# Kernel optimization log

Hardware: AMD Instinct MI355X
Metric: run time of the kernel (lower is better)

Reference implementation:

```python
import jax, jax.numpy as jnp
import numpy as np

F8_MAX = 448.0  # float8_e4m3fn max
F4_MAX = 6.0    # fp4 e2m1 max
BLOCK = 16      # NVFP4 scaling block size along K

# representable |values| of fp4 e2m1 and midpoints for nearest rounding
_LEVELS = jnp.array([0.0, 0.5, 1.0, 1.5, 2.0, 3.0, 4.0, 6.0], dtype=jnp.float32)
_MIDS = (_LEVELS[:-1] + _LEVELS[1:]) * 0.5


def _e2m1_round(a):
    # round-to-nearest fp4 e2m1 value, sign-magnitude
    s = jnp.sign(a)
    m = jnp.clip(jnp.abs(a), 0.0, F4_MAX)
    idx = jnp.searchsorted(_MIDS, m, side='left')
    return s * jnp.take(_LEVELS, idx)


def _e4m3(x):
    # quantize to float8 e4m3 and dequantize back to fp32
    return jnp.clip(x, -F8_MAX, F8_MAX).astype(jnp.float8_e4m3fn).astype(jnp.float32)


def nvfp4_fake_quant(x, s2):
    # x: [..., K]; s2: scalar global scale = 448*6/global_amax
    shp = x.shape
    K = shp[-1]
    xb = x.reshape(shp[:-1] + (K // BLOCK, BLOCK))  # [..., K/16, 16]
    amax = jnp.max(jnp.abs(xb), axis=-1, keepdims=True)
    sf = _e4m3(amax * s2 / F4_MAX)          # stored per-block fp8 scale (cutlass_vec)
    scale = sf / s2                          # per-block dequant scale in real units
    safe = jnp.where(scale > 0.0, scale, 1.0)
    q = _e2m1_round(xb / safe)               # fp4 codes (as values)
    deq = jnp.where(scale > 0.0, q * scale, 0.0)
    return deq.reshape(shp)


def setup_inputs() -> dict:
    key = jax.random.key(0)
    kx, kw, kb, ks = jax.random.split(key, 4)
    K, N = 4096, 4096
    x = jax.random.normal(kx, (4, 2048, K), dtype=jnp.float32)
    weight = jax.random.uniform(kw, (N, K), dtype=jnp.float32)
    bias = jax.random.uniform(kb, (N,), dtype=jnp.float32)
    # fp4_global_scale of a rand(1, K) tensor, as done in the module __init__
    dummy = jax.random.uniform(ks, (1, K), dtype=jnp.float32)
    s_in2 = ((F8_MAX * F4_MAX) / jnp.max(jnp.abs(dummy))).reshape(1)
    return {'x': x, 'weight': weight, 'bias': bias, 's_in2': s_in2}


def reference(x, weight, bias, s_in2):
    s2_in = s_in2.reshape(())
    s2_w = (F8_MAX * F4_MAX) / jnp.max(jnp.abs(weight))  # fp4_global_scale(weight)
    x_dq = nvfp4_fake_quant(x, s2_in)        # fake-quant activations
    w_dq = nvfp4_fake_quant(weight, s2_w)    # dequantized fp4 weight (stored at init)
    # F.linear: [b,s,k] @ [n,k]^T + bias
    return jnp.einsum('bsk,nk->bsn', x_dq, w_dq) + bias
```

## Files before the change

### kernel.cpp

```cpp
#include <hip/hip_runtime.h>
#include <hip/hip_bf16.h>

typedef __attribute__((ext_vector_type(8))) short short8;
typedef __attribute__((ext_vector_type(8))) unsigned short ushort8;
typedef __attribute__((ext_vector_type(4))) float f32x4;
typedef unsigned short ushort;

#define K_DIM 4096
#define N_DIM 4096
#define BK 64
#define NT (K_DIM / BK)


__device__ __forceinline__ float e4m3_rne(float v) {
    if (v >= 0.015625f) {
        unsigned u = __float_as_uint(v);
        unsigned lsb = (u >> 20) & 1u;
        u = (u + 0x7FFFFu + lsb) & 0xFFF00000u;
        return __uint_as_float(u);
    }
    return rintf(v * 512.0f) * 0.001953125f;
}

__device__ __forceinline__ float e2m1_level(float m) {
    float lv = 0.0f;
    lv = (m > 0.25f) ? 0.5f : lv;
    lv = (m > 0.75f) ? 1.0f : lv;
    lv = (m > 1.25f) ? 1.5f : lv;
    lv = (m > 1.75f) ? 2.0f : lv;
    lv = (m > 2.5f)  ? 3.0f : lv;
    lv = (m > 3.5f)  ? 4.0f : lv;
    lv = (m > 5.0f)  ? 6.0f : lv;
    return lv;
}

__device__ __forceinline__ ushort f32_to_bf16_bits(float f) {
    unsigned u = __float_as_uint(f);
    return (ushort)((u + 0x7FFFu + ((u >> 16) & 1u)) >> 16);
}


__global__ void wamax_kernel(const float* __restrict__ w, unsigned* amax_bits, int n4) {
    float m = 0.f;
    const f32x4* w4 = (const f32x4*)w;
    for (int i = blockIdx.x * blockDim.x + threadIdx.x; i < n4; i += gridDim.x * blockDim.x) {
        f32x4 v = w4[i];
        m = fmaxf(m, fmaxf(fmaxf(fabsf(v.x), fabsf(v.y)), fmaxf(fabsf(v.z), fabsf(v.w))));
    }
#pragma unroll
    for (int off = 32; off >= 1; off >>= 1)
        m = fmaxf(m, __shfl_down(m, off));
    __shared__ float red[4];
    const int lane = threadIdx.x & 63, wv = threadIdx.x >> 6;
    if (lane == 0) red[wv] = m;
    __syncthreads();
    if (threadIdx.x == 0) {
        m = fmaxf(fmaxf(red[0], red[1]), fmaxf(red[2], red[3]));
        atomicMax(amax_bits, __float_as_uint(m));
    }
}

__global__ void quant16_kernel(const float* __restrict__ src,
                               const float* __restrict__ s2_ptr,
                               const unsigned* __restrict__ amax_bits,
                               ushort* __restrict__ dst, int nblk) {
    int t = blockIdx.x * blockDim.x + threadIdx.x;
    if (t >= nblk) return;
    float s2;
    if (s2_ptr) s2 = *s2_ptr;
    else        s2 = 2688.0f / __uint_as_float(*amax_bits);

    const f32x4* s = (const f32x4*)src + (size_t)t * 4;
    float vals[16];
    f32x4 v0 = s[0], v1 = s[1], v2 = s[2], v3 = s[3];
#pragma unroll
    for (int i = 0; i < 4; ++i) {
        vals[i] = v0[i]; vals[4 + i] = v1[i]; vals[8 + i] = v2[i]; vals[12 + i] = v3[i];
    }
    float amax = 0.f;
#pragma unroll
    for (int i = 0; i < 16; ++i) amax = fmaxf(amax, fabsf(vals[i]));

    float sf = e4m3_rne(fminf(amax * s2 / 6.0f, 448.0f));
    float scale = sf / s2;

    ushort8 o0, o1;
    if (scale > 0.f) {
#pragma unroll
        for (int i = 0; i < 16; ++i) {
            float r = vals[i] / scale;
            float m = fminf(fabsf(r), 6.0f);
            float q = copysignf(e2m1_level(m), r);
            ushort b = f32_to_bf16_bits(q * scale);
            if (i < 8) o0[i] = b; else o1[i - 8] = b;
        }
    } else {
#pragma unroll
        for (int i = 0; i < 8; ++i) { o0[i] = 0; o1[i] = 0; }
    }
    ushort8* d8 = (ushort8*)(dst + (size_t)t * 16);
    d8[0] = o0;
    d8[1] = o1;
}


__device__ __forceinline__ void gload16(const ushort* g, ushort* l) {
    __builtin_amdgcn_global_load_lds(
        (const __attribute__((address_space(1))) void*)g,
        (__attribute__((address_space(3))) void*)l, 16, 0, 0);
}

#define VM4 asm volatile("s_waitcnt vmcnt(4)" ::: "memory")
#define VM2 asm volatile("s_waitcnt vmcnt(2)" ::: "memory")
#define VM0 asm volatile("s_waitcnt vmcnt(0)" ::: "memory")
#define BAR asm volatile("s_barrier" ::: "memory")

__global__ __launch_bounds__(512, 2) void gemm8(
    const ushort* __restrict__ Aq, const ushort* __restrict__ Bq,
    const float* __restrict__ bias, float* __restrict__ C) {
    __shared__ ushort lds[2 * 32768];

    const int tid  = threadIdx.x;
    const int lane = tid & 63;
    const int wave = tid >> 6;
    const int wr = wave >> 2;
    const int wc = wave & 3;

    const int swz = blockIdx.x;
    const int grp = swz >> 8, lcl = swz & 255;
    const int by = grp * 16 + (lcl & 15);
    const int bx = lcl >> 4;
    const int bm = by * 256, bn = bx * 256;

    const int r0  = tid >> 3;
    const int cg0 = ((tid & 7) - r0) & 7;
    const ushort* sA = Aq + (size_t)(bm + r0) * K_DIM + cg0 * 8;
    const ushort* sB = Bq + (size_t)(bn + r0) * K_DIM + cg0 * 8;
    ushort* dst0 = &lds[tid * 8];

    const int rowA = wr * 64 + (lane & 15);
    const int rowB = wc * 32 + (lane & 15);
    const int ksl  = lane >> 4;
    const int baseA[2] = { rowA * 64 + ((((ksl) + rowA) & 7) << 3),
                           rowA * 64 + (((4 + ksl + rowA) & 7) << 3) };
    const int baseB[2] = { 16384 + rowB * 64 + ((((ksl) + rowB) & 7) << 3),
                           16384 + rowB * 64 + (((4 + ksl + rowB) & 7) << 3) };

    f32x4 acc[8][4];
#pragma unroll
    for (int m = 0; m < 8; ++m)
#pragma unroll
        for (int n = 0; n < 4; ++n) acc[m][n] = (f32x4)(0.f);

    short8 af[4][2], bfr[4][2];

#define SA0(t) { const size_t ko = (size_t)(t) * BK; ushort* d = dst0 + ((t) & 1) * 32768;         \
    gload16(sA + ko, d); gload16(sA + (size_t)64 * K_DIM + ko, d + 4096); }
#define SA1(t) { const size_t ko = (size_t)(t) * BK; ushort* d = dst0 + ((t) & 1) * 32768 + 8192;  \
    gload16(sA + (size_t)128 * K_DIM + ko, d); gload16(sA + (size_t)192 * K_DIM + ko, d + 4096); }
#define SB0(t) { const size_t ko = (size_t)(t) * BK; ushort* d = dst0 + ((t) & 1) * 32768 + 16384; \
    gload16(sB + ko, d); gload16(sB + (size_t)64 * K_DIM + ko, d + 4096); }
#define SB1(t) { const size_t ko = (size_t)(t) * BK; ushort* d = dst0 + ((t) & 1) * 32768 + 24576; \
    gload16(sB + (size_t)128 * K_DIM + ko, d); gload16(sB + (size_t)192 * K_DIM + ko, d + 4096); }

#define READ_A(mh, Lb)                                                        \
    _Pragma("unroll") for (int m = 0; m < 4; ++m) {                           \
        af[m][0] = *(const short8*)((Lb) + (mh) * 8192 + m * 1024 + baseA[0]); \
        af[m][1] = *(const short8*)((Lb) + (mh) * 8192 + m * 1024 + baseA[1]); }
#define READ_B(nh, Lb)                                                        \
    _Pragma("unroll") for (int n = 0; n < 2; ++n) {                           \
        bfr[(nh)*2 + n][0] = *(const short8*)((Lb) + (nh) * 8192 + n * 1024 + baseB[0]); \
        bfr[(nh)*2 + n][1] = *(const short8*)((Lb) + (nh) * 8192 + n * 1024 + baseB[1]); }

#define MM(m0, n0)                                                            \
    __builtin_amdgcn_s_setprio(1);                                            \
    _Pragma("unroll") for (int m = 0; m < 4; ++m)                             \
    _Pragma("unroll") for (int n = 0; n < 2; ++n)                             \
    _Pragma("unroll") for (int ks = 0; ks < 2; ++ks)                          \
        acc[(m0) + m][(n0) + n] = __builtin_amdgcn_mfma_f32_16x16x32_bf16(    \
            af[m][ks], bfr[(n0) + n][ks], acc[(m0) + m][(n0) + n], 0, 0, 0);  \
    __builtin_amdgcn_s_setprio(0);

    SA0(0); SB0(0); SB1(0); SA1(0);
    VM4; BAR;

#pragma unroll 1
    for (int t = 0; t < NT - 1; ++t) {
        const ushort* Lb = &lds[(t & 1) * 32768];
        READ_A(0, Lb); READ_B(0, Lb);
        SA0(t + 1);
        VM4; BAR;
        MM(0, 0);
        BAR;
        READ_B(1, Lb);
        SB0(t + 1);
        VM4; BAR;
        MM(0, 2);
        BAR;
        READ_A(1, Lb);
        SB1(t + 1);
        BAR;
        MM(4, 0);
        BAR;
        SA1(t + 1);
        VM4; BAR;
        MM(4, 2);
        BAR;
    }
    {
        const ushort* Lb = &lds[((NT - 1) & 1) * 32768];
        READ_A(0, Lb); READ_B(0, Lb);
        VM2; BAR;
        MM(0, 0);
        BAR;
        READ_B(1, Lb);
        VM0; BAR;
        MM(0, 2);
        BAR;
        READ_A(1, Lb);
        BAR;
        MM(4, 0);
        BAR;
        BAR;
        MM(4, 2);
        BAR;
    }

    const int fq = lane >> 4, fr = lane & 15;
    const int colb = bn + wc * 32 + fr;
    float bv[4];
#pragma unroll
    for (int n = 0; n < 4; ++n) bv[n] = bias[colb + (n >> 1) * 128 + (n & 1) * 16];
#pragma unroll
    for (int m = 0; m < 8; ++m)
#pragma unroll
        for (int r = 0; r < 4; ++r) {
            const int row = bm + (m >> 2) * 128 + wr * 64 + (m & 3) * 16 + fq * 4 + r;
            float* Cr = C + (size_t)row * N_DIM + colb;
#pragma unroll
            for (int n = 0; n < 4; ++n)
                Cr[(n >> 1) * 128 + (n & 1) * 16] = acc[m][n][r] + bv[n];
        }
#undef SA0
#undef SA1
#undef SB0
#undef SB1
#undef READ_A
#undef READ_B
#undef MM
}


extern "C" void kernel_launch(void* const* d_in, const int* in_sizes, int n_in,
                              void* d_out, int out_size, void* d_ws, size_t ws_size,
                              hipStream_t stream) {
    const float* x     = (const float*)d_in[0];
    const float* w     = (const float*)d_in[1];
    const float* bias  = (const float*)d_in[2];
    const float* s_in2 = (const float*)d_in[3];
    float* out = (float*)d_out;

    const int M = in_sizes[0] / K_DIM;

    unsigned* amax_bits = (unsigned*)d_ws;
    ushort* xq = (ushort*)((char*)d_ws + 256);
    ushort* wq = (ushort*)((char*)d_ws + 256 + (size_t)M * K_DIM * 2);

    hipMemsetAsync(amax_bits, 0, 4, stream);
    wamax_kernel<<<1024, 256, 0, stream>>>(w, amax_bits, (N_DIM * K_DIM) / 4);

    const int nblk_x = (M * K_DIM) / 16;
    quant16_kernel<<<nblk_x / 256, 256, 0, stream>>>(x, s_in2, nullptr, xq, nblk_x);
    const int nblk_w = (N_DIM * K_DIM) / 16;
    quant16_kernel<<<nblk_w / 256, 256, 0, stream>>>(w, nullptr, amax_bits, wq, nblk_w);

    const int nwg = (M / 256) * (N_DIM / 256);
    gemm8<<<nwg, 512, 0, stream>>>(xq, wq, bias, out);
}
```

Before: 298.6 us.

## Double-buffer register fragments and prefetch next tile's LDS reads during MFMA

Splits A/B register fragments into separate low/high halves so the next k-tile's first fragments are read from LDS while the last MFMA quarter of the current tile runs. Replaces several full barriers with fine-grained lgkmcnt waits, which cuts the number of s_barrier stalls per iteration. This raises register pressure under the 512-thread, 2-block launch bounds. The reduced barrier set also risks LDS read/write hazards if the async global-to-LDS writes race with reads of the buffer being consumed.

```diff
diff --git a/kernel.cpp b/kernel.cpp
--- a/kernel.cpp
+++ b/kernel.cpp
@@ -113,6 +113,9 @@
 #define VM4 asm volatile("s_waitcnt vmcnt(4)" ::: "memory")
 #define VM2 asm volatile("s_waitcnt vmcnt(2)" ::: "memory")
 #define VM0 asm volatile("s_waitcnt vmcnt(0)" ::: "memory")
+#define LG4 asm volatile("s_waitcnt lgkmcnt(4)" ::: "memory")
+#define LG8 asm volatile("s_waitcnt lgkmcnt(8)" ::: "memory")
+#define LG0 asm volatile("s_waitcnt lgkmcnt(0)" ::: "memory")
 #define BAR asm volatile("s_barrier" ::: "memory")
 
 __global__ __launch_bounds__(512, 2) void gemm8(
@@ -143,8 +146,8 @@
     const int ksl  = lane >> 4;
     const int baseA[2] = { rowA * 64 + ((((ksl) + rowA) & 7) << 3),
                            rowA * 64 + (((4 + ksl + rowA) & 7) << 3) };
-    const int baseB[2] = { 16384 + rowB * 64 + ((((ksl) + rowB) & 7) << 3),
-                           16384 + rowB * 64 + (((4 + ksl + rowB) & 7) << 3) };
+    const int baseB[2] = { rowB * 64 + ((((ksl) + rowB) & 7) << 3),
+                           rowB * 64 + (((4 + ksl + rowB) & 7) << 3) };
 
     f32x4 acc[8][4];
 #pragma unroll
@@ -152,7 +155,7 @@
 #pragma unroll
         for (int n = 0; n < 4; ++n) acc[m][n] = (f32x4)(0.f);
 
-    short8 af[4][2], bfr[4][2];
+    short8 aLo[4][2], aHi[4][2], bLo[2][2], bHi[2][2];
 
 #define SA0(t) { const size_t ko = (size_t)(t) * BK; ushort* d = dst0 + ((t) & 1) * 32768;         \
     gload16(sA + ko, d); gload16(sA + (size_t)64 * K_DIM + ko, d + 4096); }
@@ -163,67 +166,70 @@
 #define SB1(t) { const size_t ko = (size_t)(t) * BK; ushort* d = dst0 + ((t) & 1) * 32768 + 24576; \
     gload16(sB + (size_t)128 * K_DIM + ko, d); gload16(sB + (size_t)192 * K_DIM + ko, d + 4096); }
 
-#define READ_A(mh, Lb)                                                        \
-    _Pragma("unroll") for (int m = 0; m < 4; ++m) {                           \
-        af[m][0] = *(const short8*)((Lb) + (mh) * 8192 + m * 1024 + baseA[0]); \
-        af[m][1] = *(const short8*)((Lb) + (mh) * 8192 + m * 1024 + baseA[1]); }
-#define READ_B(nh, Lb)                                                        \
-    _Pragma("unroll") for (int n = 0; n < 2; ++n) {                           \
-        bfr[(nh)*2 + n][0] = *(const short8*)((Lb) + (nh) * 8192 + n * 1024 + baseB[0]); \
-        bfr[(nh)*2 + n][1] = *(const short8*)((Lb) + (nh) * 8192 + n * 1024 + baseB[1]); }
-
-#define MM(m0, n0)                                                            \
+#define READ_ALO(Lb) _Pragma("unroll") for (int m = 0; m < 4; ++m) {          \
+        aLo[m][0] = *(const short8*)((Lb) + m * 1024 + baseA[0]);             \
+        aLo[m][1] = *(const short8*)((Lb) + m * 1024 + baseA[1]); }
+#define READ_AHI(Lb) _Pragma("unroll") for (int m = 0; m < 4; ++m) {          \
+        aHi[m][0] = *(const short8*)((Lb) + 8192 + m * 1024 + baseA[0]);      \
+        aHi[m][1] = *(const short8*)((Lb) + 8192 + m * 1024 + baseA[1]); }
+#define READ_BLO(Lb) _Pragma("unroll") for (int n = 0; n < 2; ++n) {          \
+        bLo[n][0] = *(const short8*)((Lb) + 16384 + n * 1024 + baseB[0]);     \
+        bLo[n][1] = *(const short8*)((Lb) + 16384 + n * 1024 + baseB[1]); }
+#define READ_BHI(Lb) _Pragma("unroll") for (int n = 0; n < 2; ++n) {          \
+        bHi[n][0] = *(const short8*)((Lb) + 24576 + n * 1024 + baseB[0]);     \
+        bHi[n][1] = *(const short8*)((Lb) + 24576 + n * 1024 + baseB[1]); }
+
+#define MMQ(AF, BF, MO, NO)                                                   \
     __builtin_amdgcn_s_setprio(1);                                            \
     _Pragma("unroll") for (int m = 0; m < 4; ++m)                             \
     _Pragma("unroll") for (int n = 0; n < 2; ++n)                             \
     _Pragma("unroll") for (int ks = 0; ks < 2; ++ks)                          \
-        acc[(m0) + m][(n0) + n] = __builtin_amdgcn_mfma_f32_16x16x32_bf16(    \
-            af[m][ks], bfr[(n0) + n][ks], acc[(m0) + m][(n0) + n], 0, 0, 0);  \
+        acc[(MO) + m][(NO) + n] = __builtin_amdgcn_mfma_f32_16x16x32_bf16(    \
+            AF[m][ks], BF[n][ks], acc[(MO) + m][(NO) + n], 0, 0, 0);          \
     __builtin_amdgcn_s_setprio(0);
 
     SA0(0); SB0(0); SB1(0); SA1(0);
     VM4; BAR;
+    {
+        const ushort* L0 = &lds[0];
+        READ_ALO(L0); READ_BLO(L0);
+    }
 
 #pragma unroll 1
     for (int t = 0; t < NT - 1; ++t) {
         const ushort* Lb = &lds[(t & 1) * 32768];
-        READ_A(0, Lb); READ_B(0, Lb);
+        const ushort* Ln = &lds[((t + 1) & 1) * 32768];
+        VM2; BAR;
+        READ_BHI(Lb);
         SA0(t + 1);
-        VM4; BAR;
-        MM(0, 0);
-        BAR;
-        READ_B(1, Lb);
+        LG4;
+        MMQ(aLo, bLo, 0, 0);
+        VM2; BAR;
+        READ_AHI(Lb);
         SB0(t + 1);
-        VM4; BAR;
-        MM(0, 2);
-        BAR;
-        READ_A(1, Lb);
+        LG8;
+        MMQ(aLo, bHi, 0, 2);
         SB1(t + 1);
-        BAR;
-        MM(4, 0);
-        BAR;
+        LG0;
+        MMQ(aHi, bLo, 4, 0);
+        VM2; BAR;
+        READ_ALO(Ln); READ_BLO(Ln);
         SA1(t + 1);
-        VM4; BAR;
-        MM(4, 2);
-        BAR;
+        MMQ(aHi, bHi, 4, 2);
     }
     {
         const ushort* Lb = &lds[((NT - 1) & 1) * 32768];
-        READ_A(0, Lb); READ_B(0, Lb);
-        VM2; BAR;
-        MM(0, 0);
-        BAR;
-        READ_B(1, Lb);
+        VM2; BAR;
+        READ_BHI(Lb);
+        LG4;
+        MMQ(aLo, bLo, 0, 0);
         VM0; BAR;
-        MM(0, 2);
-        BAR;
-        READ_A(1, Lb);
-        BAR;
-        MM(4, 0);
-        BAR;
-        BAR;
-        MM(4, 2);
-        BAR;
+        READ_AHI(Lb);
+        LG8;
+        MMQ(aLo, bHi, 0, 2);
+        LG0;
+        MMQ(aHi, bLo, 4, 0);
+        MMQ(aHi, bHi, 4, 2);
     }
 
     const int fq = lane >> 4, fr = lane & 15;
@@ -245,9 +251,11 @@
 #undef SA1
 #undef SB0
 #undef SB1
-#undef READ_A
-#undef READ_B
-#undef MM
+#undef READ_ALO
+#undef READ_AHI
+#undef READ_BLO
+#undef READ_BHI
+#undef MMQ
 }
 
 
```

Result: faster. 289.2 us (-3.2%).
